# Optimization experiments

Hardware: AMD Instinct MI355X
Metric: run time of the kernel (lower is better)

Reference implementation:

```python
import jax, jax.numpy as jnp
import numpy as np

B, N, T, H = 32, 512, 3, 8
F_IN, F_HID, F_OUT = 768, 64, 64
NEG_SLOPE = 0.2
NEG_INF = -1e9


def setup_inputs() -> dict:
    key = jax.random.key(0)
    ks = jax.random.split(key, 16)
    s = 0.05
    emb = jax.random.normal(ks[0], (B, N, F_IN), jnp.float32)
    adj = jax.random.randint(ks[1], (B, N, N), 0, 2).astype(jnp.int32)
    adj = adj.at[:, jnp.arange(N), jnp.arange(N)].set(1)  # self loops so no empty rows
    vt_idx = jax.random.randint(ks[2], (B, N), 0, T)
    v_types = jax.nn.one_hot(vt_idx, T, dtype=jnp.float32)
    # layer 1 GAT params: per-type weights [T,H,f_in,f_out]
    w1 = jax.random.normal(ks[3], (T, H, F_IN, F_HID), jnp.float32) * s
    a_src1 = jax.random.normal(ks[4], (H, F_HID), jnp.float32) * s
    a_dst1 = jax.random.normal(ks[5], (H, F_HID), jnp.float32) * s
    b1 = jnp.zeros((F_HID,), jnp.float32)
    # layer 2 GAT (single head, f_in = H*F_HID)
    w2 = jax.random.normal(ks[6], (T, 1, H * F_HID, F_OUT), jnp.float32) * s
    a_src2 = jax.random.normal(ks[7], (1, F_OUT), jnp.float32) * s
    a_dst2 = jax.random.normal(ks[8], (1, F_OUT), jnp.float32) * s
    b2 = jnp.zeros((F_OUT,), jnp.float32)
    # MLP classifier: fc1 d->3d, fc2 3d->d, fc3 d->2
    fc1_w = jax.random.normal(ks[9], (F_OUT, 3 * F_OUT), jnp.float32) * s
    fc1_b = jnp.zeros((3 * F_OUT,), jnp.float32)
    fc2_w = jax.random.normal(ks[10], (3 * F_OUT, F_OUT), jnp.float32) * s
    fc2_b = jnp.zeros((F_OUT,), jnp.float32)
    fc3_w = jax.random.normal(ks[11], (F_OUT, 2), jnp.float32) * s
    fc3_b = jnp.zeros((2,), jnp.float32)
    return dict(emb=emb, adj=adj, v_types=v_types,
                w1=w1, a_src1=a_src1, a_dst1=a_dst1, b1=b1,
                w2=w2, a_src2=a_src2, a_dst2=a_dst2, b2=b2,
                fc1_w=fc1_w, fc1_b=fc1_b, fc2_w=fc2_w, fc2_b=fc2_b,
                fc3_w=fc3_w, fc3_b=fc3_b)


def _leaky_relu(x):
    return jnp.where(x >= 0, x, NEG_SLOPE * x)


def _gat(h, adj_mask, vt, w, a_src, a_dst, bias):
    # h: [B,N,f_in], vt: [B,N,T] one-hot, w: [T,Hd,f_in,f_out]
    # per-type projection then select node's type
    hpt = jnp.einsum('bni,thio->bntho', h, w)          # [B,N,T,Hd,f_out]
    hp = jnp.einsum('bnt,bntho->bnho', vt, hpt)        # [B,N,Hd,f_out]
    src = jnp.einsum('bnho,ho->bhn', hp, a_src)        # [B,Hd,N]
    dst = jnp.einsum('bnho,ho->bhn', hp, a_dst)
    e = _leaky_relu(src[:, :, :, None] + dst[:, :, None, :])  # [B,Hd,N,N]
    e = jnp.where(adj_mask[:, None, :, :], e, NEG_INF)
    attn = jax.nn.softmax(e, axis=-1)                  # attn_dropout=0.0 -> identity
    out = jnp.einsum('bhnm,bmho->bhno', attn, hp) + bias
    return out                                         # [B,Hd,N,f_out]


def reference(emb, adj, v_types, w1, a_src1, a_dst1, b1,
              w2, a_src2, a_dst2, b2,
              fc1_w, fc1_b, fc2_w, fc2_b, fc3_w, fc3_b):
    adj_mask = adj > 0
    x = _gat(emb, adj_mask, v_types, w1, a_src1, a_dst1, b1)    # [B,H,N,F_HID]
    x = jnp.transpose(x, (0, 2, 1, 3)).reshape(B, N, H * F_HID)  # concat heads
    x = jax.nn.elu(x)                                            # dropout: eval mode (identity)
    x = _gat(x, adj_mask, v_types, w2, a_src2, a_dst2, b2)       # [B,1,N,F_OUT]
    x = jax.nn.elu(x)
    x = x[:, 0, :, :]                                            # squeeze head dim -> [B,N,F_OUT]
    left = x[:, 0, :]
    right = x[:, 1, :]
    v = left * right
    v = jax.nn.relu(v @ fc1_w + fc1_b)
    v = jax.nn.relu(v @ fc2_w + fc2_b)
    scores = v @ fc3_w + fc3_b
    return jax.nn.log_softmax(scores, axis=1)
```

## Files before the change

kernel.cpp:

```cpp
#include <hip/hip_runtime.h>

#define BB   32
#define NN   512
#define NH   8
#define FIN  768
#define FHID 64
#define NROWS (BB*NN)

typedef __attribute__((ext_vector_type(8))) short bf16x8;
typedef __attribute__((ext_vector_type(4))) short s16x4;
typedef __attribute__((ext_vector_type(4))) float f32x4;
typedef unsigned long long u64;
typedef unsigned short u16;

__device__ __forceinline__ float lrelu_f(float s){ return fmaxf(s, 0.2f*s); }
__device__ __forceinline__ float elu_f(float s){ return s > 0.f ? s : expm1f(s); }
__device__ __forceinline__ short f2bf(float f){
  unsigned u = __float_as_uint(f);
  return (short)((u + 0x7fffu + ((u >> 16) & 1u)) >> 16);
}
__device__ __forceinline__ float bf2f(short s){
  return __uint_as_float(((unsigned)(u16)s) << 16);
}

__global__ __launch_bounds__(256) void prep_kernel(
    const int* __restrict__ adj,
    u64* __restrict__ maskw)
{
  int row  = blockIdx.x * 4 + (threadIdx.x >> 6);
  int lane = threadIdx.x & 63;
  const int* arow = adj + (long)row * NN;
  #pragma unroll
  for (int w = 0; w < 8; ++w) {
    u64 bal = __ballot(arow[w*64 + lane] > 0);
    if (lane == 0) maskw[(long)row*8 + w] = bal;
  }
}

__global__ __launch_bounds__(256) void rowlist_kernel(
    const float* __restrict__ vt,
    int* __restrict__ rowlist, int* __restrict__ counts)
{
  __shared__ int lc[3];
  __shared__ int lbase[3];
  int tid = threadIdx.x;
  int row = blockIdx.x * 256 + tid;
  if (tid < 3) lc[tid] = 0;
  __syncthreads();
  const float* v = vt + (long)row*3;
  int t = v[1] > 0.5f ? 1 : (v[2] > 0.5f ? 2 : 0);
  int p = atomicAdd(&lc[t], 1);
  __syncthreads();
  if (tid < 3) lbase[tid] = atomicAdd(&counts[tid], lc[tid]);
  __syncthreads();
  rowlist[t*NROWS + lbase[t] + p] = row;
}

__global__ __launch_bounds__(256) void conv_w(
    const float* __restrict__ w1, const float* __restrict__ w2,
    u16* __restrict__ w1t, u16* __restrict__ w2t)
{
  __shared__ float tile[64][68];
  int bid = blockIdx.x, tid = threadIdx.x;
  const float* src; u16* dst; int K;
  if (bid < 24) { src = w1 + (long)bid*768*64; dst = w1t + (long)bid*64*768; K = 768; }
  else { int t = bid - 24; src = w2 + (long)t*512*64; dst = w2t + (long)t*64*512; K = 512; }
  int kq = blockIdx.y;
  int kstart = kq * (K >> 2), kend = kstart + (K >> 2);

  for (int k0 = kstart; k0 < kend; k0 += 64) {
    __syncthreads();
    #pragma unroll
    for (int i = 0; i < 4; ++i) {
      int kk = i*16 + (tid >> 4);
      int oo = (tid & 15) * 4;
      float4 v = *(const float4*)(src + (long)(k0 + kk)*64 + oo);
      *(float4*)&tile[kk][oo] = v;
    }
    __syncthreads();
    int o = tid >> 2, kp = (tid & 3) * 16;
    bf16x8 r0, r1;
    #pragma unroll
    for (int j = 0; j < 8; ++j) r0[j] = f2bf(tile[kp + j][o]);
    #pragma unroll
    for (int j = 0; j < 8; ++j) r1[j] = f2bf(tile[kp + 8 + j][o]);
    u16* d = dst + (long)o*K + k0 + kp;
    *(bf16x8*)d = r0;
    *(bf16x8*)(d + 8) = r1;
  }
}

__global__ __launch_bounds__(256) void gemm1_mfma(
    const float* __restrict__ emb,
    const u16* __restrict__ w1t,
    const int* __restrict__ rowlist, const int* __restrict__ counts,
    u16* __restrict__ hp1b)
{
  int t   = blockIdx.z;
  int cnt = counts[t];
  int i   = blockIdx.x;
  int xcd = i & 7;
  int q   = i >> 3;
  int hb  = q & 3;
  int rb  = (q >> 2) * 8 + xcd;
  int r0  = rb * 64;
  if (r0 >= cnt) return;

  __shared__ short aT[4*66*8];
  __shared__ short bT[4*130*8];
  __shared__ int rowsS[64];

  int tid = threadIdx.x;
  if (tid < 64) {
    int rr = r0 + tid;
    rowsS[tid] = (rr < cnt) ? rowlist[t*NROWS + rr] : -1;
  }
  __syncthreads();

  int ar = tid >> 2, ac = tid & 3;
  int sg = rowsS[ar]; if (sg < 0) sg = rowsS[0];
  const float* aP = emb + (long)sg*768;

  int colb = tid >> 2, off = tid & 3;
  const u16* bP1 = w1t + (((long)t*8 + hb*2 + 0)*64 + colb)*768;
  const u16* bP2 = w1t + (((long)t*8 + hb*2 + 1)*64 + colb)*768;

  int wv = tid >> 6, l = tid & 63;
  int wr = wv >> 1, wc = wv & 1;
  int l15 = l & 15, lg = l >> 4;

  f32x4 acc[2][4];
  #pragma unroll
  for (int fr = 0; fr < 2; ++fr)
    #pragma unroll
    for (int cf = 0; cf < 4; ++cf) acc[fr][cf] = (f32x4){0.f,0.f,0.f,0.f};

  float4 ra0 = *(const float4*)(aP + ac*4);
  float4 ra1 = *(const float4*)(aP + 16 + ac*4);
  bf16x8 rb1 = *(const bf16x8*)(bP1 + off*8);
  bf16x8 rb2 = *(const bf16x8*)(bP2 + off*8);

  for (int k0 = 0; k0 < 768; k0 += 32) {
    __syncthreads();
    s16x4 w0, w1;
    w0[0]=f2bf(ra0.x); w0[1]=f2bf(ra0.y); w0[2]=f2bf(ra0.z); w0[3]=f2bf(ra0.w);
    w1[0]=f2bf(ra1.x); w1[1]=f2bf(ra1.y); w1[2]=f2bf(ra1.z); w1[3]=f2bf(ra1.w);
    *(s16x4*)&aT[(( (ac>>1)     )*66 + ar)*8 + (ac&1)*4] = w0;
    *(s16x4*)&aT[(( 2 + (ac>>1) )*66 + ar)*8 + (ac&1)*4] = w1;
    *(bf16x8*)&bT[(off*130 + colb     )*8] = rb1;
    *(bf16x8*)&bT[(off*130 + colb + 64)*8] = rb2;
    __syncthreads();
    if (k0 + 32 < 768) {
      ra0 = *(const float4*)(aP + k0 + 32 + ac*4);
      ra1 = *(const float4*)(aP + k0 + 48 + ac*4);
      rb1 = *(const bf16x8*)(bP1 + k0 + 32 + off*8);
      rb2 = *(const bf16x8*)(bP2 + k0 + 32 + off*8);
    }
    bf16x8 af[2], bfr[4];
    #pragma unroll
    for (int fr = 0; fr < 2; ++fr)
      af[fr] = *(const bf16x8*)&aT[(lg*66 + wr*32 + fr*16 + l15)*8];
    #pragma unroll
    for (int cf = 0; cf < 4; ++cf)
      bfr[cf] = *(const bf16x8*)&bT[(lg*130 + wc*64 + cf*16 + l15)*8];
    #pragma unroll
    for (int fr = 0; fr < 2; ++fr)
      #pragma unroll
      for (int cf = 0; cf < 4; ++cf)
        acc[fr][cf] = __builtin_amdgcn_mfma_f32_16x16x32_bf16(af[fr], bfr[cf], acc[fr][cf], 0, 0, 0);
  }

  #pragma unroll
  for (int fr = 0; fr < 2; ++fr) {
    #pragma unroll
    for (int r = 0; r < 4; ++r) {
      int rloc = wr*32 + fr*16 + lg*4 + r;
      int rg = rowsS[rloc];
      if (rg < 0) continue;
      long obase = ((long)(rg >> 9) * 8) * 32768 + (long)(rg & 511) * 64;
      #pragma unroll
      for (int cf = 0; cf < 4; ++cf) {
        int c = wc*64 + cf*16 + l15;
        hp1b[obase + (long)(hb*2 + (c >> 6))*32768 + (c & 63)] = (u16)f2bf(acc[fr][cf][r]);
      }
    }
  }
}

__global__ __launch_bounds__(256) void gemm2_mfma(
    const u16* __restrict__ xbf,
    const u16* __restrict__ w2t,
    const int* __restrict__ rowlist, const int* __restrict__ counts,
    float* __restrict__ hp2)
{
  int t   = blockIdx.z;
  int cnt = counts[t];
  int r0  = blockIdx.y * 64;
  if (r0 >= cnt) return;

  __shared__ short aT[4*66*8];
  __shared__ short bT[4*66*8];
  __shared__ int rowsS[64];

  int tid = threadIdx.x;
  if (tid < 64) {
    int rr = r0 + tid;
    rowsS[tid] = (rr < cnt) ? rowlist[t*NROWS + rr] : -1;
  }
  __syncthreads();

  int ar = tid >> 2, ac = tid & 3;
  int sg = rowsS[ar]; if (sg < 0) sg = rowsS[0];
  long apart = ((long)(sg >> 9) * 8) * 32768 + (long)(sg & 511) * 64;

  int colb = tid >> 2, off = tid & 3;
  const u16* bP = w2t + ((long)t*64 + colb)*512;

  int wv = tid >> 6, l = tid & 63;
  int l15 = l & 15, lg = l >> 4;

  f32x4 acc[4];
  #pragma unroll
  for (int cf = 0; cf < 4; ++cf) acc[cf] = (f32x4){0.f,0.f,0.f,0.f};

  int ka0 = ac*8;
  bf16x8 ra = *(const bf16x8*)(xbf + apart + (long)(ka0 >> 6)*32768 + (ka0 & 63));
  bf16x8 rb = *(const bf16x8*)(bP + off*8);

  for (int k0 = 0; k0 < 512; k0 += 32) {
    __syncthreads();
    *(bf16x8*)&aT[(ac*66 + ar)*8]   = ra;
    *(bf16x8*)&bT[(off*66 + colb)*8] = rb;
    __syncthreads();
    if (k0 + 32 < 512) {
      int kn = k0 + 32 + ac*8;
      ra = *(const bf16x8*)(xbf + apart + (long)(kn >> 6)*32768 + (kn & 63));
      rb = *(const bf16x8*)(bP + k0 + 32 + off*8);
    }
    bf16x8 af, bfr[4];
    af = *(const bf16x8*)&aT[(lg*66 + wv*16 + l15)*8];
    #pragma unroll
    for (int cf = 0; cf < 4; ++cf)
      bfr[cf] = *(const bf16x8*)&bT[(lg*66 + cf*16 + l15)*8];
    #pragma unroll
    for (int cf = 0; cf < 4; ++cf)
      acc[cf] = __builtin_amdgcn_mfma_f32_16x16x32_bf16(af, bfr[cf], acc[cf], 0, 0, 0);
  }

  #pragma unroll
  for (int r = 0; r < 4; ++r) {
    int rloc = wv*16 + lg*4 + r;
    int rg = rowsS[rloc];
    if (rg < 0) continue;
    #pragma unroll
    for (int cf = 0; cf < 4; ++cf)
      hp2[(long)rg*64 + cf*16 + l15] = acc[cf][r];
  }
}

__global__ __launch_bounds__(1024) void gat1_attn(
    u16* __restrict__ hp1b, const u64* __restrict__ maskw,
    const float* __restrict__ a_src, const float* __restrict__ a_dst,
    const float* __restrict__ b1)
{
  extern __shared__ char smc[];
  short* hpTf = (short*)smc;
  short* pSf  = (short*)(smc + 67584);
  float* srcS = (float*)(smc + 135168);
  float* dstS = (float*)(smc + 137216);
  float* asS  = (float*)(smc + 139264);
  float* adS  = (float*)(smc + 139520);
  float* rcpS = (float*)(smc + 139776);

  int bh = blockIdx.x;
  int b = bh >> 3, h = bh & 7;
  int tid = threadIdx.x;

  if (tid < 64) asS[tid] = a_src[h*64 + tid];
  else if (tid < 128) adS[tid - 64] = a_dst[h*64 + (tid - 64)];
  __syncthreads();

  {
    int m = tid >> 1, half = tid & 1;
    int koct = m >> 3, sub = m & 7;
    const u16* hpRow = hp1b + ((long)bh*NN + m)*64 + half*32;
    float ps = 0.f, pd = 0.f;
    #pragma unroll
    for (int qq = 0; qq < 4; ++qq) {
      bf16x8 hv = *(const bf16x8*)(hpRow + qq*8);
      int o0 = half*32 + qq*8;
      #pragma unroll
      for (int j = 0; j < 8; ++j) {
        float f = bf2f(hv[j]);
        ps += f * asS[o0 + j];
        pd += f * adS[o0 + j];
        hpTf[(koct*66 + o0 + j)*8 + sub] = hv[j];
      }
    }
    ps += __shfl_xor(ps, 1);
    pd += __shfl_xor(pd, 1);
    if ((tid & 1) == 0) { srcS[m] = ps; dstS[m] = pd; }
  }
  __syncthreads();

  int wv = tid >> 6, lane = tid & 63;
  int l15 = lane & 15, lg = lane >> 4;
  int cgl = wv >> 2, nt = wv & 3;
  int lk = lane >> 3, ls = lane & 7;
  int o_out = nt*16 + l15;
  float bb  = b1[o_out];

  for (int sup = 0; sup < 8; ++sup) {
    #pragma unroll
    for (int rr = 0; rr < 4; ++rr) {
      int rloc = wv*4 + rr;
      int row  = sup*64 + rloc;
      float srcv = srcS[row];
      const u64* mrow = maskw + ((long)(b*NN + row))*8;
      float lsum = 0.f;
      #pragma unroll
      for (int j = 0; j < 8; ++j) {
        u64 w = mrow[j];
        float s = srcv + dstS[j*64 + lane];
        float e = ((w >> lane) & 1ull) ? lrelu_f(s) : -1.0e9f;
        float p = __expf(e);
        lsum += p;
        pSf[((j*8 + lk)*66 + rloc)*8 + ls] = f2bf(p);
      }
      #pragma unroll
      for (int mk = 1; mk <= 32; mk <<= 1) lsum += __shfl_xor(lsum, mk);
      if (lane == 0) rcpS[rloc] = 1.f / lsum;
    }
    __syncthreads();

    f32x4 acc = {0.f, 0.f, 0.f, 0.f};
    #pragma unroll
    for (int ks = 0; ks < 16; ++ks) {
      int koct = ks*4 + lg;
      bf16x8 af = *(const bf16x8*)&pSf [(koct*66 + cgl*16 + l15)*8];
      bf16x8 bf = *(const bf16x8*)&hpTf[(koct*66 + nt*16  + l15)*8];
      acc = __builtin_amdgcn_mfma_f32_16x16x32_bf16(af, bf, acc, 0, 0, 0);
    }
    #pragma unroll
    for (int reg = 0; reg < 4; ++reg) {
      int rloc = cgl*16 + lg*4 + reg;
      int row  = sup*64 + rloc;
      float v = elu_f(acc[reg] * rcpS[rloc] + bb);
      hp1b[((long)bh*NN + row)*64 + o_out] = (u16)f2bf(v);
    }
    __syncthreads();
  }
}

__global__ __launch_bounds__(256) void gat2_final(
    const float* __restrict__ hp2, const u64* __restrict__ maskw,
    const float* __restrict__ a_src2, const float* __restrict__ a_dst2,
    const float* __restrict__ b2,
    const float* __restrict__ fc1_w, const float* __restrict__ fc1_b,
    const float* __restrict__ fc2_w, const float* __restrict__ fc2_b,
    const float* __restrict__ fc3_w, const float* __restrict__ fc3_b,
    float* __restrict__ out)
{
  extern __shared__ float sm[];
  float* hpS  = sm;
  float* dstS = hpS + 32768;
  float* srcS = dstS + 512;
  float* pS   = srcS + 512;
  float* redS = pS + 512;
  float* outS = redS + 256;
  float* vS   = outS + 128;
  float* y1S  = vS + 64;
  float* redM = y1S + 192;
  float4* hpS4 = (float4*)hpS;

  int b = blockIdx.x;
  int tid = threadIdx.x;
  int og = tid & 15, m16 = tid >> 4;

  for (int it = 0; it < 32; ++it) {
    int fi = it*256 + tid;
    int m = fi >> 4, o4 = fi & 15;
    hpS4[m*16 + o4] = *(const float4*)(hp2 + (long)(b*NN + m)*64 + o4*4);
  }
  __syncthreads();

  float4 as4 = *(const float4*)(a_src2 + og*4);
  float4 ad4 = *(const float4*)(a_dst2 + og*4);
  for (int it = 0; it < 32; ++it) {
    int m = it*16 + m16;
    float4 hv = hpS4[m*16 + og];
    float ls = hv.x*as4.x + hv.y*as4.y + hv.z*as4.z + hv.w*as4.w;
    float ld = hv.x*ad4.x + hv.y*ad4.y + hv.z*ad4.z + hv.w*ad4.w;
    #pragma unroll
    for (int mk = 1; mk <= 8; mk <<= 1) {
      ls += __shfl_xor(ls, mk);
      ld += __shfl_xor(ld, mk);
    }
    if (og == 0) { srcS[m] = ls; dstS[m] = ld; }
  }
  __syncthreads();

  for (int n = 0; n < 2; ++n) {
    float srcv = srcS[n];
    const u64* mrow = maskw + (long)(b*NN + n)*8;
    int m0 = tid, m1 = tid + 256;
    u64 w0 = mrow[m0 >> 6], w1 = mrow[m1 >> 6];
    float s0 = srcv + dstS[m0], s1 = srcv + dstS[m1];
    float e0 = ((w0 >> (m0 & 63)) & 1ull) ? lrelu_f(s0) : -1.0e9f;
    float e1 = ((w1 >> (m1 & 63)) & 1ull) ? lrelu_f(s1) : -1.0e9f;
    float emax = fmaxf(e0, e1);
    #pragma unroll
    for (int mk = 1; mk <= 32; mk <<= 1) emax = fmaxf(emax, __shfl_xor(emax, mk));
    if ((tid & 63) == 0) redM[tid >> 6] = emax;
    __syncthreads();
    emax = fmaxf(fmaxf(redM[0], redM[1]), fmaxf(redM[2], redM[3]));
    float p0 = __expf(e0 - emax), p1 = __expf(e1 - emax);
    pS[m0] = p0; pS[m1] = p1;
    float lsum = p0 + p1;
    #pragma unroll
    for (int mk = 1; mk <= 32; mk <<= 1) lsum += __shfl_xor(lsum, mk);
    if ((tid & 63) == 0) redM[4 + (tid >> 6)] = lsum;
    __syncthreads();
    float rcp = 1.f / (redM[4] + redM[5] + redM[6] + redM[7]);

    float4 acc = make_float4(0.f,0.f,0.f,0.f);
    for (int mm = 0; mm < 32; ++mm) {
      int m = mm*16 + m16;
      float4 hv = hpS4[m*16 + og];
      float p = pS[m];
      acc.x += hv.x*p; acc.y += hv.y*p; acc.z += hv.z*p; acc.w += hv.w*p;
    }
    acc.x += __shfl_xor(acc.x, 16); acc.y += __shfl_xor(acc.y, 16);
    acc.z += __shfl_xor(acc.z, 16); acc.w += __shfl_xor(acc.w, 16);
    acc.x += __shfl_xor(acc.x, 32); acc.y += __shfl_xor(acc.y, 32);
    acc.z += __shfl_xor(acc.z, 32); acc.w += __shfl_xor(acc.w, 32);
    __syncthreads();
    if ((tid & 63) < 16) ((float4*)redS)[(tid >> 6)*16 + (tid & 15)] = acc;
    __syncthreads();
    if (tid < 16) {
      float4 s = make_float4(0.f,0.f,0.f,0.f);
      #pragma unroll
      for (int w = 0; w < 4; ++w) {
        float4 v = ((float4*)redS)[w*16 + tid];
        s.x += v.x; s.y += v.y; s.z += v.z; s.w += v.w;
      }
      float4 bv = *(const float4*)(b2 + tid*4);
      outS[n*64 + tid*4 + 0] = elu_f(s.x*rcp + bv.x);
      outS[n*64 + tid*4 + 1] = elu_f(s.y*rcp + bv.y);
      outS[n*64 + tid*4 + 2] = elu_f(s.z*rcp + bv.z);
      outS[n*64 + tid*4 + 3] = elu_f(s.w*rcp + bv.w);
    }
    __syncthreads();
  }

  if (tid < 64) vS[tid] = outS[tid] * outS[64 + tid];
  __syncthreads();
  if (tid < 192) {
    float a = fc1_b[tid];
    for (int o = 0; o < 64; ++o) a += vS[o]*fc1_w[o*192 + tid];
    y1S[tid] = a > 0.f ? a : 0.f;
  }
  __syncthreads();
  if (tid < 64) {
    float a = fc2_b[tid];
    for (int j = 0; j < 192; ++j) a += y1S[j]*fc2_w[j*64 + tid];
    vS[tid] = a > 0.f ? a : 0.f;
  }
  __syncthreads();
  if (tid == 0) {
    float t0 = fc3_b[0], t1 = fc3_b[1];
    for (int k = 0; k < 64; ++k) {
      float y = vS[k];
      t0 += y*fc3_w[k*2 + 0];
      t1 += y*fc3_w[k*2 + 1];
    }
    float mx = fmaxf(t0, t1);
    float lse = mx + logf(__expf(t0 - mx) + __expf(t1 - mx));
    out[b*2 + 0] = t0 - lse;
    out[b*2 + 1] = t1 - lse;
  }
}

extern "C" void kernel_launch(void* const* d_in, const int* in_sizes, int n_in,
                              void* d_out, int out_size, void* d_ws, size_t ws_size,
                              hipStream_t stream) {
  const float* emb    = (const float*)d_in[0];
  const int*   adj    = (const int*)d_in[1];
  const float* vt     = (const float*)d_in[2];
  const float* w1     = (const float*)d_in[3];
  const float* a_src1 = (const float*)d_in[4];
  const float* a_dst1 = (const float*)d_in[5];
  const float* b1     = (const float*)d_in[6];
  const float* w2     = (const float*)d_in[7];
  const float* a_src2 = (const float*)d_in[8];
  const float* a_dst2 = (const float*)d_in[9];
  const float* b2     = (const float*)d_in[10];
  const float* fc1_w  = (const float*)d_in[11];
  const float* fc1_b  = (const float*)d_in[12];
  const float* fc2_w  = (const float*)d_in[13];
  const float* fc2_b  = (const float*)d_in[14];
  const float* fc3_w  = (const float*)d_in[15];
  const float* fc3_b  = (const float*)d_in[16];

  char* ws = (char*)d_ws;
  int* counts  = (int*)ws;
  int* rowlist = (int*)(ws + 4096);
  u64* maskw   = (u64*)(ws + 204800);
  u16* w1t     = (u16*)(ws + 1310720);
  u16* w2t     = (u16*)(ws + 3670016);
  u16* hp1b    = (u16*)(ws + 3932160);
  float* hp2   = (float*)(ws + 20709376);

  hipMemsetAsync(counts, 0, 16, stream);
  prep_kernel<<<NROWS/4, 256, 0, stream>>>(adj, maskw);
  rowlist_kernel<<<NROWS/256, 256, 0, stream>>>(vt, rowlist, counts);
  conv_w<<<dim3(27, 4), 256, 0, stream>>>(w1, w2, w1t, w2t);

  gemm1_mfma<<<dim3(352, 1, 3), 256, 0, stream>>>(emb, w1t, rowlist, counts, hp1b);

  size_t sm1 = 140032;
  gat1_attn<<<BB*NH, 1024, sm1, stream>>>(hp1b, maskw, a_src1, a_dst1, b1);

  gemm2_mfma<<<dim3(1, 256, 3), 256, 0, stream>>>(hp1b, w2t, rowlist, counts, hp2);

  size_t sm2 = (size_t)(32768 + 512 + 512 + 512 + 256 + 128 + 64 + 192 + 8) * 4;
  gat2_final<<<BB, 256, sm2, stream>>>(hp2, maskw, a_src2, a_dst2, b2,
                                       fc1_w, fc1_b, fc2_w, fc2_b, fc3_w, fc3_b,
                                       (float*)d_out);
}
```

Baseline: 158.9 us.

## Software-pipeline gat1 softmax with MFMA via register staging and double-buffered reciprocals

In the layer-1 attention kernel, the softmax probabilities for the next 64-row block are now computed into registers while the MFMA aggregation of the current block runs. They are written to shared memory only after a barrier. The reciprocal row sums are double-buffered, which adds 256 bytes of shared memory. The dst scores are hoisted into registers, and fp32 to bf16 packing now uses the v_cvt_pk_bf16_f32 instruction. The aim is to overlap exp/mask work with matrix cores. The cost is more register pressure in a 1024-thread block and an extra barrier per iteration.

```diff
diff --git a/kernel.cpp b/kernel.cpp
--- a/kernel.cpp
+++ b/kernel.cpp
@@ -21,6 +21,11 @@
 }
 __device__ __forceinline__ float bf2f(short s){
   return __uint_as_float(((unsigned)(u16)s) << 16);
+}
+__device__ __forceinline__ unsigned cvt_pk_bf16(float lo, float hi){
+  unsigned r;
+  asm("v_cvt_pk_bf16_f32 %0, %1, %2" : "=v"(r) : "v"(lo), "v"(hi));
+  return r;
 }
 
 __global__ __launch_bounds__(256) void prep_kernel(
@@ -258,6 +263,52 @@
   }
 }
 
+__device__ __forceinline__ void softmax_rows(
+    int b, int sup, int wv, int lane,
+    const u64* __restrict__ maskw, const float* srcS, const float (&dstv)[8],
+    float* rcpDst, unsigned (&pk)[4][4])
+{
+  #pragma unroll
+  for (int rr = 0; rr < 4; ++rr) {
+    int rloc = wv*4 + rr;
+    int row  = sup*64 + rloc;
+    float srcv = srcS[row];
+    const u64* mrow = maskw + ((long)(b*NN + row))*8;
+    float ev[8];
+    float lsum = 0.f;
+    #pragma unroll
+    for (int j = 0; j < 8; ++j) {
+      u64 w = mrow[j];
+      float s = srcv + dstv[j];
+      float e = ((w >> lane) & 1ull) ? lrelu_f(s) : -1.0e9f;
+      float p = __expf(e);
+      lsum += p;
+      ev[j] = p;
+    }
+    #pragma unroll
+    for (int mk = 1; mk <= 32; mk <<= 1) lsum += __shfl_xor(lsum, mk);
+    if (lane == 0) rcpDst[rloc] = 1.f / lsum;
+    #pragma unroll
+    for (int qq = 0; qq < 4; ++qq)
+      pk[rr][qq] = cvt_pk_bf16(ev[2*qq], ev[2*qq+1]);
+  }
+}
+
+__device__ __forceinline__ void write_pk(
+    short* pSf, int wv, int lk, int ls, const unsigned (&pk)[4][4])
+{
+  #pragma unroll
+  for (int rr = 0; rr < 4; ++rr) {
+    int rloc = wv*4 + rr;
+    #pragma unroll
+    for (int qq = 0; qq < 4; ++qq) {
+      unsigned v = pk[rr][qq];
+      pSf[(((2*qq    )*8 + lk)*66 + rloc)*8 + ls] = (short)(v & 0xffffu);
+      pSf[(((2*qq + 1)*8 + lk)*66 + rloc)*8 + ls] = (short)(v >> 16);
+    }
+  }
+}
+
 __global__ __launch_bounds__(1024) void gat1_attn(
     u16* __restrict__ hp1b, const u64* __restrict__ maskw,
     const float* __restrict__ a_src, const float* __restrict__ a_dst,
@@ -310,28 +361,22 @@
   int o_out = nt*16 + l15;
   float bb  = b1[o_out];
 
+  float dstv[8];
+  #pragma unroll
+  for (int j = 0; j < 8; ++j) dstv[j] = dstS[j*64 + lane];
+
+  {
+    unsigned pk0[4][4];
+    softmax_rows(b, 0, wv, lane, maskw, srcS, dstv, rcpS, pk0);
+    write_pk(pSf, wv, lk, ls, pk0);
+  }
+  __syncthreads();
+
   for (int sup = 0; sup < 8; ++sup) {
-    #pragma unroll
-    for (int rr = 0; rr < 4; ++rr) {
-      int rloc = wv*4 + rr;
-      int row  = sup*64 + rloc;
-      float srcv = srcS[row];
-      const u64* mrow = maskw + ((long)(b*NN + row))*8;
-      float lsum = 0.f;
-      #pragma unroll
-      for (int j = 0; j < 8; ++j) {
-        u64 w = mrow[j];
-        float s = srcv + dstS[j*64 + lane];
-        float e = ((w >> lane) & 1ull) ? lrelu_f(s) : -1.0e9f;
-        float p = __expf(e);
-        lsum += p;
-        pSf[((j*8 + lk)*66 + rloc)*8 + ls] = f2bf(p);
-      }
-      #pragma unroll
-      for (int mk = 1; mk <= 32; mk <<= 1) lsum += __shfl_xor(lsum, mk);
-      if (lane == 0) rcpS[rloc] = 1.f / lsum;
-    }
-    __syncthreads();
+    unsigned pk2[4][4];
+    if (sup < 7)
+      softmax_rows(b, sup + 1, wv, lane, maskw, srcS, dstv,
+                   rcpS + ((sup + 1) & 1)*64, pk2);
 
     f32x4 acc = {0.f, 0.f, 0.f, 0.f};
     #pragma unroll
@@ -341,13 +386,16 @@
       bf16x8 bf = *(const bf16x8*)&hpTf[(koct*66 + nt*16  + l15)*8];
       acc = __builtin_amdgcn_mfma_f32_16x16x32_bf16(af, bf, acc, 0, 0, 0);
     }
+    const float* rcpCur = rcpS + (sup & 1)*64;
     #pragma unroll
     for (int reg = 0; reg < 4; ++reg) {
       int rloc = cgl*16 + lg*4 + reg;
       int row  = sup*64 + rloc;
-      float v = elu_f(acc[reg] * rcpS[rloc] + bb);
+      float v = elu_f(acc[reg] * rcpCur[rloc] + bb);
       hp1b[((long)bh*NN + row)*64 + o_out] = (u16)f2bf(v);
     }
+    __syncthreads();
+    if (sup < 7) write_pk(pSf, wv, lk, ls, pk2);
     __syncthreads();
   }
 }
@@ -518,7 +566,7 @@
 
   gemm1_mfma<<<dim3(352, 1, 3), 256, 0, stream>>>(emb, w1t, rowlist, counts, hp1b);
 
-  size_t sm1 = 140032;
+  size_t sm1 = 140288;
   gat1_attn<<<BB*NH, 1024, sm1, stream>>>(hp1b, maskw, a_src1, a_dst1, b1);
 
   gemm2_mfma<<<dim3(1, 256, 3), 256, 0, stream>>>(hp1b, w2t, rowlist, counts, hp2);
```

New measurement: 171.2 us. 7.7% more time.
